# Kernel optimization log

Hardware: AMD Instinct MI355X
Metric: run time of the kernel (lower is better)

## Reference

```python
import jax, jax.numpy as jnp
import numpy as np

K = 1.0          # Lorentz curvature param: x_t^2 - |x_s|^2 = K
SQRT_K = 1.0
EPS = 1e-8
HEADS = 12

def add_time(s):
    t = jnp.sqrt(K + jnp.sum(s * s, axis=-1, keepdims=True))
    return jnp.concatenate([t, s], axis=-1)

def lorentz_ln(x, g, b):
    s = x[..., 1:]
    mu = jnp.mean(s, axis=-1, keepdims=True)
    var = jnp.var(s, axis=-1, keepdims=True)
    s = (s - mu) / jnp.sqrt(var + 1e-5) * g + b
    return add_time(s)

def lorentz_fc(x, W, heads=None, act=None):
    # linear on full Lorentz vector -> space part; time recomputed to stay on manifold
    s = x @ W.T
    if act is not None:
        s = act(s)
    if heads is not None:
        bsz, n, dt = s.shape
        s = s.reshape(bsz, n, heads, dt // heads).transpose(0, 2, 1, 3)  # (b,h,n,hd)
    return add_time(s)

def logmap0(x):
    t, s = x[..., :1], x[..., 1:]
    sn = jnp.sqrt(jnp.sum(s * s, axis=-1, keepdims=True))
    dist = SQRT_K * jnp.arccosh(jnp.maximum(t / SQRT_K, 1.0 + 1e-7))
    u = dist * s / jnp.maximum(sn, EPS)
    return jnp.concatenate([jnp.zeros_like(t), u], axis=-1)

def expmap0(u):
    us = u[..., 1:]
    n = jnp.sqrt(jnp.sum(us * us, axis=-1, keepdims=True))
    nc = jnp.maximum(n, EPS)
    t = SQRT_K * jnp.cosh(n / SQRT_K)
    s = SQRT_K * jnp.sinh(n / SQRT_K) * us / nc
    return jnp.concatenate([t, s], axis=-1)

def ste_clip(x, lo, hi):
    # straight-through estimator: clamp in fwd, identity grad
    return x + jax.lax.stop_gradient(jnp.clip(x, lo, hi) - x)

def ste_max_clamp(x, hi):
    return x + jax.lax.stop_gradient(jnp.minimum(x, hi) - x)

def mha_last_layer(x, Wq, Wk, Wv, Wo, alpha_raw, tau_raw, lambda_raw):
    q = lorentz_fc(x, Wq, heads=HEADS)   # (b,h,n,hd+1)
    k = lorentz_fc(x, Wk, heads=HEADS)
    v = lorentz_fc(x, Wv, heads=HEADS)
    q_t, q_s = q[..., :1], q[..., 1:]
    k_t, k_s = k[..., :1], k[..., 1:]
    # Lorentzian inner product -> hyperbolic pairwise distances
    inner_QK = -q_t @ jnp.swapaxes(k_t, -1, -2) + jnp.einsum('bhid,bhjd->bhij', q_s, k_s)
    raw_cosh = jnp.maximum(-inner_QK / K, 1.0)                # (b,h,n,n)
    is_self = raw_cosh < 1.0 + 1e-5
    safe_cosh = jnp.where(is_self, 2.0, raw_cosh)
    dist_QK = SQRT_K * jnp.arccosh(safe_cosh)
    cosh_OQ = jnp.maximum(q_t / SQRT_K, 1.0 + 1e-7)
    cosh_OK = jnp.maximum(k_t / SQRT_K, 1.0 + 1e-7)
    c_tilde = jnp.minimum(SQRT_K * jnp.arccosh(cosh_OQ), 40.0) / SQRT_K  # (b,h,n,1)
    sinh_QK = jnp.sinh(dist_QK / SQRT_K)
    sinh_OQ = jnp.sinh(c_tilde)
    numer = raw_cosh * cosh_OQ - jnp.swapaxes(cosh_OK, -1, -2)
    raw_Z = numer / (sinh_OQ * sinh_QK)
    Z_safe = jnp.where(is_self, 1.0, ste_clip(raw_Z, -1.0, 1.0))
    alpha = jax.nn.softplus(alpha_raw)
    B = alpha * c_tilde / (1.0 + alpha * c_tilde)
    lam = jax.nn.softplus(lambda_raw)
    d_L = ste_max_clamp(dist_QK, 40.0)   # float32 branch of STE_Dist_Clamp
    log_dist_penalty = -lam * jnp.log1p(d_L * d_L)
    m = 0.1
    entail = jax.nn.softplus(B + Z_safe - m) - jax.nn.softplus(jnp.asarray(-m, B.dtype))
    tau = jax.nn.softplus(tau_raw)
    score = jax.nn.softmax(log_dist_penalty - tau * entail, axis=-1)
    # expmap aggregation: tangent-space weighted mean
    v_tan = logmap0(v)
    agg = jnp.einsum('bhij,bhjd->bhid', score, v_tan)
    agg = agg / (jnp.sum(score, axis=-1, keepdims=True) + 1e-8)
    attn = expmap0(agg).transpose(0, 2, 1, 3)   # (b,n,h,hd+1)
    bsz, n, h, _ = attn.shape
    attn_s = attn[..., 1:].reshape(bsz, n, -1)
    attn_t = attn[..., :1].reshape(bsz, n, -1)
    t_new = jnp.sqrt(jnp.sum(attn_t ** 2, axis=-1, keepdims=True) - (h - 1) * K)
    return lorentz_fc(jnp.concatenate([t_new, attn_s], axis=-1), Wo)


def setup_inputs() -> dict:
    key = jax.random.key(0)
    ks = jax.random.split(key, 8)
    b, n, hidden, mlp_hidden = 4, 1024, 769, 3073
    d = hidden - 1
    xs = jax.random.normal(ks[0], (b, n, d), jnp.float32)
    x = add_time(xs)
    def w(k, o, i):
        return jax.random.normal(k, (o, i), jnp.float32) * (i ** -0.5)
    return {
        'x': x,
        'Wq': w(ks[1], d, hidden), 'Wk': w(ks[2], d, hidden), 'Wv': w(ks[3], d, hidden),
        'Wo': w(ks[4], d, hidden),
        'ln1_g': jnp.ones((d,), jnp.float32), 'ln1_b': jnp.zeros((d,), jnp.float32),
        'ln2_g': jnp.ones((d,), jnp.float32), 'ln2_b': jnp.zeros((d,), jnp.float32),
        'Wm1': w(ks[5], mlp_hidden - 1, hidden), 'Wm2': w(ks[6], d, mlp_hidden),
        'alpha_raw': jnp.zeros((1,), jnp.float32),
        'tau_raw': jnp.zeros((1,), jnp.float32),
        'lambda_raw': jnp.zeros((1,), jnp.float32),
    }


def reference(x, Wq, Wk, Wv, Wo, ln1_g, ln1_b, ln2_g, ln2_b, Wm1, Wm2, alpha_raw, tau_raw, lambda_raw):
    out = mha_last_layer(lorentz_ln(x, ln1_g, ln1_b), Wq, Wk, Wv, Wo, alpha_raw, tau_raw, lambda_raw)
    out = out[..., 1:] + x[..., 1:]                 # residual on space part (DropPath=identity in eval)
    h = lorentz_ln(add_time(out), ln2_g, ln2_b)
    h = lorentz_fc(h, Wm1, act=lambda z: jax.nn.gelu(z, approximate=False))
    h = lorentz_fc(h, Wm2)
    out = h[..., 1:] + out
    return add_time(out)
```

## Files before the change

kernel.cpp:

```cpp
#include <hip/hip_runtime.h>
#include <cstdint>
#include <cstddef>

typedef unsigned short u16;
typedef __attribute__((ext_vector_type(8))) __bf16 bf16x8;
typedef __attribute__((ext_vector_type(4))) float f32x4;
typedef __attribute__((ext_vector_type(4))) short s16x4;

#define SEQ 1024
#define MROWS 4096
#define DDIM 768
#define HID 769
#define KP1 800
#define MLPD 3072
#define KP2 3104
#define NHEADS 12
#define LN2F 0.69314718056f
#define LOG2EF 1.44269504089f

static __device__ __forceinline__ u16 f2bf(float f){
  union { float f; uint32_t u; } v; v.f = f;
  return (u16)((v.u + 0x7FFFu + ((v.u >> 16) & 1u)) >> 16);
}

static __device__ __forceinline__ f32x4 mfma16(bf16x8 a, bf16x8 b, f32x4 c){
  return __builtin_amdgcn_mfma_f32_16x16x32_bf16(a, b, c, 0, 0, 0);
}

static __device__ __forceinline__ f32x4 mfma16k(s16x4 a, s16x4 b, f32x4 c){
  return __builtin_amdgcn_mfma_f32_16x16x16bf16_1k(a, b, c, 0, 0, 0);
}

static __device__ __forceinline__ s16x4 pack4(uint32_t lo, uint32_t hi){
  union { uint2 u; s16x4 v; } cv; cv.u.x = lo; cv.u.y = hi; return cv.v;
}

static __device__ __forceinline__ void async_lds16(const u16* g, u16* l){
  u16* gm = const_cast<u16*>(g);
  __builtin_amdgcn_global_load_lds(
      (__attribute__((address_space(1))) void*)gm,
      (__attribute__((address_space(3))) void*)l, 16, 0, 0);
}

static __device__ __forceinline__ float blk_reduce(float v, float* red, int tid){
  #pragma unroll
  for (int off = 1; off < 64; off <<= 1) v += __shfl_xor(v, off, 64);
  __syncthreads();
  if ((tid & 63) == 0) red[tid >> 6] = v;
  __syncthreads();
  return red[0] + red[1] + red[2] + red[3];
}

static __device__ __forceinline__ float gelu_fast(float z){
  float z2 = z * z;
  float t = __builtin_fmaf(z2, 0.044715f, 1.f);
  float w = z * t * (-2.3022078f);
  float e2 = __builtin_amdgcn_exp2f(w);
  return z * __builtin_amdgcn_rcpf(1.f + e2);
}

static __device__ __forceinline__ void conv_seg(const float* W, u16* O, int idx, int K, int Kp){
  int n = idx / Kp, k = idx - n * Kp;
  O[idx] = (k < K) ? f2bf(W[(size_t)n * K + k]) : (u16)0;
}
__global__ __launch_bounds__(256) void conv_all(const float* __restrict__ Wq, const float* __restrict__ Wk,
    const float* __restrict__ Wv, const float* __restrict__ Wo,
    const float* __restrict__ Wm1, const float* __restrict__ Wm2, u16* __restrict__ dst){
  int b = blockIdx.x, tid = threadIdx.x;
  if (b < 2400){        conv_seg(Wq,  dst,            b*256+tid,        769, 800); }
  else if (b < 4800){   conv_seg(Wk,  dst + 614400,  (b-2400)*256+tid,  769, 800); }
  else if (b < 7200){   conv_seg(Wv,  dst + 1228800, (b-4800)*256+tid,  769, 800); }
  else if (b < 9600){   conv_seg(Wo,  dst + 1843200, (b-7200)*256+tid,  769, 800); }
  else if (b < 19200){  conv_seg(Wm1, dst + 2457600, (b-9600)*256+tid,  769, 800); }
  else {                conv_seg(Wm2, dst + 4915200, (b-19200)*256+tid, 3073, 3104); }
}

__global__ __launch_bounds__(256) void ln_kernel(const float* __restrict__ X, int xstr, int xoff,
    const float* __restrict__ g, const float* __restrict__ b, u16* __restrict__ O){
  __shared__ float red[4];
  int m = blockIdx.x, tid = threadIdx.x;
  const float* xr = X + (size_t)m * xstr + xoff;
  float s[3], y[3];
  float s1 = 0.f, s2 = 0.f;
  #pragma unroll
  for (int j = 0; j < 3; j++){ float v = xr[tid + j*256]; s[j] = v; s1 += v; s2 += v*v; }
  s1 = blk_reduce(s1, red, tid);
  s2 = blk_reduce(s2, red, tid);
  float mu = s1 * (1.f/768.f);
  float var = s2 * (1.f/768.f) - mu*mu;
  float rstd = rsqrtf(var + 1e-5f);
  float q = 0.f;
  #pragma unroll
  for (int j = 0; j < 3; j++){ int i = tid + j*256; y[j] = (s[j]-mu)*rstd*g[i] + b[i]; q += y[j]*y[j]; }
  q = blk_reduce(q, red, tid);
  u16* orow = O + (size_t)m * KP1;
  #pragma unroll
  for (int j = 0; j < 3; j++) orow[1 + tid + j*256] = f2bf(y[j]);
  if (tid == 0) orow[0] = f2bf(sqrtf(1.f + q));
  if (tid < 31) orow[769 + tid] = 0;
}

__global__ __launch_bounds__(256) void ln_sum_kernel(const float* __restrict__ P2,
    const float* __restrict__ x, const float* __restrict__ g, const float* __restrict__ b,
    float* __restrict__ out1, u16* __restrict__ O, float* __restrict__ rsq){
  __shared__ float red[4];
  int m = blockIdx.x, tid = threadIdx.x;
  if (tid == 0) rsq[m] = 0.f;
  float s[3], y[3];
  float s1 = 0.f, s2 = 0.f;
  #pragma unroll
  for (int j = 0; j < 3; j++){
    int col = tid + j*256;
    float v = x[(size_t)m * HID + 1 + col];
    #pragma unroll
    for (int z = 0; z < 2; z++) v += P2[(size_t)z*MROWS*DDIM + (size_t)m*DDIM + col];
    out1[(size_t)m*DDIM + col] = v;
    s[j] = v; s1 += v; s2 += v*v;
  }
  s1 = blk_reduce(s1, red, tid);
  s2 = blk_reduce(s2, red, tid);
  float mu = s1 * (1.f/768.f);
  float var = s2 * (1.f/768.f) - mu*mu;
  float rstd = rsqrtf(var + 1e-5f);
  float q = 0.f;
  #pragma unroll
  for (int j = 0; j < 3; j++){ int i = tid + j*256; y[j] = (s[j]-mu)*rstd*g[i] + b[i]; q += y[j]*y[j]; }
  q = blk_reduce(q, red, tid);
  u16* orow = O + (size_t)m * KP1;
  #pragma unroll
  for (int j = 0; j < 3; j++) orow[1 + tid + j*256] = f2bf(y[j]);
  if (tid == 0) orow[0] = f2bf(sqrtf(1.f + q));
  if (tid < 31) orow[769 + tid] = 0;
}

__global__ __launch_bounds__(256) void gemm_split(
    const u16* __restrict__ A, const u16* __restrict__ B, float* __restrict__ C,
    int N, int Kp)
{
  __shared__ u16 As[128*32];
  __shared__ u16 Bs[128*32];
  int tid = threadIdx.x;
  int wave = tid >> 6, lane = tid & 63;
  int lrow = lane & 15, lq = lane >> 4;
  int m0 = blockIdx.y * 128, n0 = blockIdx.x * 128;
  int wm = wave >> 1, wn = wave & 1;
  int chunks = Kp >> 5;
  int nz = gridDim.z, z = blockIdx.z;
  int base = chunks / nz, rem = chunks - base * nz;
  int begin = z * base + (z < rem ? z : rem);
  int count = base + (z < rem ? 1 : 0);
  C += (size_t)z * MROWS * N;
  f32x4 acc[4][4] = {};
  int seg = wave * 2;
  int srow = lane >> 2;
  int scol = (lane & 3) * 8;
  const u16* Abase = A + (size_t)m0 * Kp;
  const u16* Bbase = B + (size_t)n0 * Kp;
  for (int kc = begin; kc < begin + count; kc++){
    int k0 = kc * 32;
    __syncthreads();
    #pragma unroll
    for (int i = 0; i < 2; i++){
      int s = seg + i;
      async_lds16(Abase + (size_t)(s*16 + srow) * Kp + k0 + scol, As + s*512);
      async_lds16(Bbase + (size_t)(s*16 + srow) * Kp + k0 + scol, Bs + s*512);
    }
    __syncthreads();
    bf16x8 af[4], bfr[4];
    #pragma unroll
    for (int t = 0; t < 4; t++){
      af[t]  = *(const bf16x8*)(As + (wm*64 + t*16 + lrow)*32 + lq*8);
      bfr[t] = *(const bf16x8*)(Bs + (wn*64 + t*16 + lrow)*32 + lq*8);
    }
    #pragma unroll
    for (int mt = 0; mt < 4; mt++)
      #pragma unroll
      for (int nt = 0; nt < 4; nt++)
        acc[mt][nt] = mfma16(af[mt], bfr[nt], acc[mt][nt]);
  }
  #pragma unroll
  for (int mt = 0; mt < 4; mt++)
    #pragma unroll
    for (int nt = 0; nt < 4; nt++){
      int col = n0 + wn*64 + nt*16 + lrow;
      #pragma unroll
      for (int r = 0; r < 4; r++){
        int row = m0 + wm*64 + mt*16 + lq*4 + r;
        C[(size_t)row * N + col] = acc[mt][nt][r];
      }
    }
}

__global__ __launch_bounds__(256) void gemm64(
    const u16* __restrict__ A, const u16* __restrict__ B,
    float* __restrict__ C, u16* __restrict__ Og, float* __restrict__ rsq,
    int N, int Kp, int gelu)
{
  __shared__ u16 As[128*32];
  __shared__ u16 Bs[64*32];
  int tid = threadIdx.x;
  int wave = tid >> 6, lane = tid & 63;
  int lrow = lane & 15, lq = lane >> 4;
  int m0 = blockIdx.y * 128, n0 = blockIdx.x * 64;
  int wm = wave >> 1, wn = wave & 1;
  int chunks = Kp >> 5;
  int nz = gridDim.z, z = blockIdx.z;
  int base = chunks / nz, rem = chunks - base * nz;
  int begin = z * base + (z < rem ? z : rem);
  int count = base + (z < rem ? 1 : 0);
  f32x4 acc[4][2] = {};
  int srow = lane >> 2;
  int scol = (lane & 3) * 8;
  const u16* Abase = A + (size_t)m0 * Kp;
  const u16* Bbase = B + (size_t)n0 * Kp;
  for (int kc = begin; kc < begin + count; kc++){
    int k0 = kc * 32;
    __syncthreads();
    #pragma unroll
    for (int i = 0; i < 2; i++){
      int s = wave*2 + i;
      async_lds16(Abase + (size_t)(s*16 + srow) * Kp + k0 + scol, As + s*512);
    }
    async_lds16(Bbase + (size_t)(wave*16 + srow) * Kp + k0 + scol, Bs + wave*512);
    __syncthreads();
    bf16x8 af[4], bfr[2];
    #pragma unroll
    for (int t = 0; t < 4; t++)
      af[t]  = *(const bf16x8*)(As + (wm*64 + t*16 + lrow)*32 + lq*8);
    #pragma unroll
    for (int t = 0; t < 2; t++)
      bfr[t] = *(const bf16x8*)(Bs + (wn*32 + t*16 + lrow)*32 + lq*8);
    #pragma unroll
    for (int mt = 0; mt < 4; mt++)
      #pragma unroll
      for (int nt = 0; nt < 2; nt++)
        acc[mt][nt] = mfma16(af[mt], bfr[nt], acc[mt][nt]);
  }
  if (gelu == 0){
    C += (size_t)z * MROWS * N;
    #pragma unroll
    for (int mt = 0; mt < 4; mt++)
      #pragma unroll
      for (int nt = 0; nt < 2; nt++){
        int col = n0 + wn*32 + nt*16 + lrow;
        #pragma unroll
        for (int r = 0; r < 4; r++){
          int row = m0 + wm*64 + mt*16 + lq*4 + r;
          C[(size_t)row * N + col] = acc[mt][nt][r];
        }
      }
  } else {
    float ssq[4][4];
    #pragma unroll
    for (int mt = 0; mt < 4; mt++)
      #pragma unroll
      for (int r = 0; r < 4; r++) ssq[mt][r] = 0.f;
    #pragma unroll
    for (int mt = 0; mt < 4; mt++)
      #pragma unroll
      for (int nt = 0; nt < 2; nt++){
        int col = n0 + wn*32 + nt*16 + lrow;
        #pragma unroll
        for (int r = 0; r < 4; r++){
          int row = m0 + wm*64 + mt*16 + lq*4 + r;
          float e = gelu_fast(acc[mt][nt][r]);
          ssq[mt][r] += e*e;
          Og[(size_t)row * KP2 + 1 + col] = f2bf(e);
        }
      }
    #pragma unroll
    for (int mt = 0; mt < 4; mt++)
      #pragma unroll
      for (int r = 0; r < 4; r++){
        float v = ssq[mt][r];
        v += __shfl_xor(v, 1, 64);
        v += __shfl_xor(v, 2, 64);
        v += __shfl_xor(v, 4, 64);
        v += __shfl_xor(v, 8, 64);
        if (lrow == 0)
          atomicAdd(rsq + m0 + wm*64 + mt*16 + lq*4 + r, v);
      }
  }
}

__global__ __launch_bounds__(256) void timecol(const float* __restrict__ rsq, u16* __restrict__ O){
  int idx = blockIdx.x * 256 + threadIdx.x;
  int m = idx >> 5, j = idx & 31;
  if (j == 0) O[(size_t)m * KP2] = f2bf(sqrtf(1.f + rsq[m]));
  else        O[(size_t)m * KP2 + 3072 + j] = 0;
}

__global__ __launch_bounds__(256) void pack_qk(const float* __restrict__ raw,
    u16* __restrict__ Qp, u16* __restrict__ Kpk, float* __restrict__ qt, float* __restrict__ kt)
{
  int wave = threadIdx.x >> 6, lane = threadIdx.x & 63;
  int m = blockIdx.x * 4 + wave;
  int h = blockIdx.y;
  int which = blockIdx.z;
  const float* src = raw + (size_t)m * 2304 + which * 768 + h*64 + lane;
  float v = *src;
  float ss = v*v;
  #pragma unroll
  for (int off = 1; off < 64; off <<= 1) ss += __shfl_xor(ss, off, 64);
  int b = m >> 10, n = m & 1023, bh = b * NHEADS + h;
  u16* dst = (which ? Kpk : Qp) + ((size_t)bh * SEQ + n) * 64 + lane;
  *dst = f2bf(v);
  if (lane == 0) (which ? kt : qt)[bh * SEQ + n] = sqrtf(1.f + ss);
}

__global__ __launch_bounds__(256) void pack_v(const float* __restrict__ vraw, u16* __restrict__ Vf){
  __shared__ float part[256];
  __shared__ float scl[64];
  __shared__ float tile[64][65];
  int tid = threadIdx.x;
  int kb = blockIdx.x, bh = blockIdx.y;
  int b = bh / NHEADS, h = bh - b*NHEADS;
  int kl = tid >> 2;
  int d0 = (tid & 3) * 16;
  int m = b * SEQ + kb * 64 + kl;
  float v[16]; float ss = 0.f;
  const float* src = vraw + (size_t)m * 2304 + h*64 + d0;
  #pragma unroll
  for (int i = 0; i < 16; i++){ v[i] = src[i]; ss += v[i]*v[i]; }
  part[tid] = ss;
  __syncthreads();
  if ((tid & 3) == 0){
    float s2 = part[tid] + part[tid+1] + part[tid+2] + part[tid+3];
    float sn = sqrtf(s2);
    float tv = sqrtf(1.f + s2);
    float ctv = fmaxf(tv, 1.f + 1e-7f);
    float dist = __logf(ctv + sqrtf(fmaxf(ctv*ctv - 1.f, 0.f)));
    scl[kl] = dist / fmaxf(sn, 1e-8f);
  }
  __syncthreads();
  float sc = scl[kl];
  #pragma unroll
  for (int i = 0; i < 16; i++) tile[kl][d0 + i] = v[i] * sc;
  __syncthreads();
  #pragma unroll
  for (int i = 0; i < 2; i++){
    int idx = tid + i*256;
    int ctg_l = idx >> 7;
    int ntp = (idx >> 6) & 1;
    int ln  = idx & 63;
    int lr = ln & 15, lqq = ln >> 4;
    int k0 = ctg_l*16 + lqq*4;
    int dlo = ntp*32 + lr;
    u16 tmp[8];
    #pragma unroll
    for (int j = 0; j < 4; j++){
      tmp[j]     = f2bf(tile[k0+j][dlo]);
      tmp[4+j]   = f2bf(tile[k0+j][dlo+16]);
    }
    u16* dst = Vf + ((((size_t)bh*64 + kb*4 + ctg_l)*2 + ntp)*64 + ln)*8;
    *(uint4*)dst = *(const uint4*)tmp;
  }
}

__global__ __launch_bounds__(256) void attn_kernel(
    const u16* __restrict__ Q, const u16* __restrict__ K, const u16* __restrict__ Vf,
    const float* __restrict__ qt, const float* __restrict__ kt,
    float* __restrict__ pAgg, float* __restrict__ pDen,
    const float* __restrict__ a_raw, const float* __restrict__ t_raw, const float* __restrict__ l_raw)
{
  __shared__ float rv[4][64];
  int tid = threadIdx.x;
  int bh = blockIdx.y, ks = blockIdx.z;
  int qbase = blockIdx.x * 64;
  float alpha = __logf(1.f + __expf(a_raw[0]));
  float tau   = __logf(1.f + __expf(t_raw[0]));
  float lam   = __logf(1.f + __expf(l_raw[0]));
  if (tid < 64){
    float qtv = qt[bh * SEQ + qbase + tid];
    float cq = fmaxf(qtv, 1.f + 1e-7f);
    float A = cq + __builtin_amdgcn_sqrtf(fmaxf(cq*cq - 1.f, 0.f));
    float ct = fminf(__builtin_amdgcn_logf(A) * LN2F, 40.f);
    float e = __expf(ct);
    float sh = 0.5f * (e - __builtin_amdgcn_rcpf(e));
    float ac = alpha * ct;
    rv[0][tid] = qtv;
    rv[1][tid] = cq;
    rv[2][tid] = __builtin_amdgcn_rcpf(sh);
    rv[3][tid] = (ac * __builtin_amdgcn_rcpf(1.f + ac) - 0.1f) * LOG2EF;
  }
  __syncthreads();
  int wave = tid >> 6, lane = tid & 63;
  int lrow = lane & 15, lq = lane >> 4;
  int myrow = wave*16 + lrow;
  float qt_l = rv[0][myrow], cq_l = rv[1][myrow], rri_l = rv[2][myrow], Bw_l = rv[3][myrow];
  const float tbase = tau * 0.92967051f;
  const u16* Qb = Q + ((size_t)bh * SEQ + qbase + wave*16 + lrow) * 64 + lq*8;
  bf16x8 bq0 = *(const bf16x8*)Qb;
  bf16x8 bq1 = *(const bf16x8*)(Qb + 32);
  const u16* Kt = K + (size_t)bh * SEQ * 64 + (size_t)(ks*512 + lrow) * 64 + lq*8;
  const u16* Vp = Vf + (size_t)bh * 65536 + (size_t)(ks*32) * 1024 + lane*8;
  const float* ktp = kt + (size_t)bh * SEQ + ks*512 + lq*4;
  s16x4 ones;
  ones[0] = (short)0x3F80; ones[1] = (short)0x3F80; ones[2] = (short)0x3F80; ones[3] = (short)0x3F80;
  f32x4 o[4] = {};
  f32x4 dacc = {};
  for (int jt = 0; jt < 8; jt++){
    bf16x8 vv[8];
    #pragma unroll
    for (int ct = 0; ct < 4; ct++){
      vv[ct*2]   = *(const bf16x8*)(Vp + ct*1024);
      vv[ct*2+1] = *(const bf16x8*)(Vp + ct*1024 + 512);
    }
    float4 kv[4];
    #pragma unroll
    for (int ct = 0; ct < 4; ct++) kv[ct] = *(const float4*)(ktp + ct*16);
    f32x4 s[4];
    #pragma unroll
    for (int ct = 0; ct < 4; ct++){
      bf16x8 a0 = *(const bf16x8*)(Kt + ct*1024);
      bf16x8 a1 = *(const bf16x8*)(Kt + ct*1024 + 32);
      f32x4 z = {0.f, 0.f, 0.f, 0.f};
      z = mfma16(a0, bq0, z);
      z = mfma16(a1, bq1, z);
      s[ct] = z;
    }
    #pragma unroll
    for (int ct = 0; ct < 4; ct++){
      float4 kvv = kv[ct];
      uint32_t pu[4];
      #pragma unroll
      for (int r = 0; r < 4; r++){
        float ktv = (r == 0) ? kvv.x : (r == 1) ? kvv.y : (r == 2) ? kvv.z : kvv.w;
        float c = fmaxf(__builtin_fmaf(qt_l, ktv, -s[ct][r]), 1.f);
        bool self = c < 1.00001f;
        float ce = self ? 2.f : c;
        float cm1 = __builtin_fmaf(ce, ce, -1.f);
        float rs = __builtin_amdgcn_rsqf(cm1);
        float shq = cm1 * rs;
        float d = __builtin_amdgcn_logf(ce + shq) * LN2F;
        float L1 = __builtin_amdgcn_logf(__builtin_fmaf(d, d, 1.f));
        float Z = __builtin_fmaf(ce, cq_l, -ktv) * rri_l * rs;
        Z = fminf(fmaxf(Z, -1.f), 1.f);
        Z = self ? 1.f : Z;
        float w2 = __builtin_fmaf(Z, LOG2EF, Bw_l);
        float ew = __builtin_amdgcn_exp2f(w2);
        float L2 = __builtin_amdgcn_logf(ew + 1.f);
        float logit = __builtin_fmaf(-lam, L1, __builtin_fmaf(-tau, L2, tbase));
        float p = __builtin_amdgcn_exp2f(logit);
        pu[r] = __float_as_uint(p);
      }
      uint32_t lo = __builtin_amdgcn_perm(pu[1], pu[0], 0x07060302u);
      uint32_t hi = __builtin_amdgcn_perm(pu[3], pu[2], 0x07060302u);
      s16x4 pb = pack4(lo, hi);
      union { bf16x8 v8; s16x4 h[2]; } c0, c1;
      c0.v8 = vv[ct*2]; c1.v8 = vv[ct*2+1];
      o[0] = mfma16k(c0.h[0], pb, o[0]);
      o[1] = mfma16k(c0.h[1], pb, o[1]);
      o[2] = mfma16k(c1.h[0], pb, o[2]);
      o[3] = mfma16k(c1.h[1], pb, o[3]);
      dacc = mfma16k(ones, pb, dacc);
    }
    Kt += 4096; Vp += 4096; ktp += 64;
  }
  size_t rowb = (size_t)(ks*48 + bh) * SEQ + qbase + wave*16 + lrow;
  if (lq == 0) pDen[rowb] = dacc[0];
  #pragma unroll
  for (int nt = 0; nt < 4; nt++){
    float4 ov; ov.x = o[nt][0]; ov.y = o[nt][1]; ov.z = o[nt][2]; ov.w = o[nt][3];
    *(float4*)(pAgg + rowb * 64 + nt*16 + lq*4) = ov;
  }
}

__global__ __launch_bounds__(768) void expmap_pack(const float* __restrict__ pAgg,
    const float* __restrict__ pDen, u16* __restrict__ O){
  __shared__ float th2[NHEADS];
  int m = blockIdx.x, tid = threadIdx.x;
  int h = tid >> 6, lane = tid & 63;
  int b = m >> 10, n = m & 1023, bh = b*NHEADS + h;
  size_t i0 = ((size_t)bh * SEQ + n);
  size_t i1 = ((size_t)(48 + bh) * SEQ + n);
  float d = pDen[i0] + pDen[i1];
  float rden = __builtin_amdgcn_rcpf(d * (1.f + 1e-8f));
  float u = (pAgg[i0*64 + lane] + pAgg[i1*64 + lane]) * rden;
  float n2 = u*u;
  #pragma unroll
  for (int off = 1; off < 64; off <<= 1) n2 += __shfl_xor(n2, off, 64);
  float nn = sqrtf(n2);
  float e = __expf(nn);
  float ch = 0.5f * (e + 1.f/e);
  float sh = 0.5f * (e - 1.f/e);
  float sc = sh / fmaxf(nn, 1e-8f);
  u16* orow = O + (size_t)m * KP1;
  orow[1 + h*64 + lane] = f2bf(u * sc);
  if (lane == 0) th2[h] = ch*ch;
  __syncthreads();
  if (tid == 0){
    float ssum = 0.f;
    #pragma unroll
    for (int i = 0; i < NHEADS; i++) ssum += th2[i];
    orow[0] = f2bf(sqrtf(ssum - 11.f));
  }
  if (tid >= 1 && tid < 32) orow[768 + tid] = 0;
}

__global__ __launch_bounds__(256) void final_sum(const float* __restrict__ P4,
    const float* __restrict__ out1, float* __restrict__ out){
  __shared__ float red[4];
  int m = blockIdx.x, tid = threadIdx.x;
  float v[3]; float s2 = 0.f;
  #pragma unroll
  for (int j = 0; j < 3; j++){
    int col = tid + j*256;
    float t = out1[(size_t)m*DDIM + col];
    #pragma unroll
    for (int z = 0; z < 4; z++) t += P4[(size_t)z*MROWS*DDIM + (size_t)m*DDIM + col];
    v[j] = t; s2 += t*t;
  }
  s2 = blk_reduce(s2, red, tid);
  float* orow = out + (size_t)m * HID;
  if (tid == 0) orow[0] = sqrtf(1.f + s2);
  #pragma unroll
  for (int j = 0; j < 3; j++) orow[1 + tid + j*256] = v[j];
}

extern "C" void kernel_launch(void* const* d_in, const int* in_sizes, int n_in,
                              void* d_out, int out_size, void* d_ws, size_t ws_size,
                              hipStream_t stream)
{
  (void)in_sizes; (void)n_in; (void)out_size; (void)ws_size;
  const float* x   = (const float*)d_in[0];
  const float* Wq  = (const float*)d_in[1];
  const float* Wk  = (const float*)d_in[2];
  const float* Wv  = (const float*)d_in[3];
  const float* Wo  = (const float*)d_in[4];
  const float* g1p = (const float*)d_in[5];
  const float* b1p = (const float*)d_in[6];
  const float* g2p = (const float*)d_in[7];
  const float* b2p = (const float*)d_in[8];
  const float* Wm1 = (const float*)d_in[9];
  const float* Wm2 = (const float*)d_in[10];
  const float* ar  = (const float*)d_in[11];
  const float* tr  = (const float*)d_in[12];
  const float* lr  = (const float*)d_in[13];

  char* ws = (char*)d_ws;
  u16*   wqb  = (u16*)(ws + 0);
  u16*   wob  = (u16*)(ws + 3686400);
  u16*   wm1b = (u16*)(ws + 4915200);
  u16*   wm2b = (u16*)(ws + 9830400);
  u16*   xln  = (u16*)(ws + 14598144);
  float* qkv  = (float*)(ws + 21151744);
  u16*   qp   = (u16*)(ws + 58900480);
  u16*   kpk  = (u16*)(ws + 65191936);
  u16*   vf   = (u16*)(ws + 71483392);
  float* rsq  = (float*)(ws + 77774848);
  float* qtb  = (float*)(ws + 77791232);
  float* ktb  = (float*)(ws + 77987840);
  float* pAgg = (float*)(ws + 78381056);
  float* pDen = (float*)(ws + 103546880);
  u16*   woin = (u16*)(ws + 103940096);
  float* woP  = (float*)(ws + 21151744);
  float* out1 = (float*)(ws + 103940096);
  u16*   ln2b = (u16*)(ws + 78381056);
  u16*   g1b  = (u16*)(ws + 21151744);
  float* out2P= (float*)(ws + 46579712);

  conv_all<<<dim3(28512), 256, 0, stream>>>(Wq, Wk, Wv, Wo, Wm1, Wm2, wqb);
  ln_kernel<<<dim3(4096), 256, 0, stream>>>(x, 769, 1, g1p, b1p, xln);
  gemm64<<<dim3(36, 32, 1), 256, 0, stream>>>(xln, wqb, qkv, nullptr, nullptr, 2304, 800, 0);
  pack_qk<<<dim3(1024, 12, 2), 256, 0, stream>>>(qkv, qp, kpk, qtb, ktb);
  pack_v<<<dim3(16, 48), 256, 0, stream>>>(qkv + 1536, vf);
  attn_kernel<<<dim3(16, 48, 2), 256, 0, stream>>>(qp, kpk, vf, qtb, ktb, pAgg, pDen, ar, tr, lr);
  expmap_pack<<<dim3(4096), 768, 0, stream>>>(pAgg, pDen, woin);
  gemm64<<<dim3(12, 32, 2), 256, 0, stream>>>(woin, wob, woP, nullptr, nullptr, 768, 800, 0);
  ln_sum_kernel<<<dim3(4096), 256, 0, stream>>>(woP, x, g2p, b2p, out1, ln2b, rsq);
  gemm64<<<dim3(48, 32, 1), 256, 0, stream>>>(ln2b, wm1b, nullptr, g1b, rsq, 3072, 800, 1);
  timecol<<<dim3(512), 256, 0, stream>>>(rsq, g1b);
  gemm_split<<<dim3(6, 32, 4), 256, 0, stream>>>(g1b, wm2b, out2P, 768, 3104);
  final_sum<<<dim3(4096), 256, 0, stream>>>(out2P, out1, (float*)d_out);
}
```

Measured before the change: 393.6 us.

## Deepen GEMM K-tile to 64 and reuse gemm64 for MLP down-projection

The gemm64 kernel now stages 64-wide K chunks per iteration instead of 32, which halves the number of barrier pairs and doubles the MFMA work between syncs. All padded K dimensions grow to multiples of 64 (832 and 3136), with the padding writes and workspace offsets adjusted to match. The separate 128x128 gemm_split kernel is removed, and the final MLP GEMM now runs on gemm64 with 64-wide N tiles and a 4-way K split. The cost is extra zero-padding work, double the shared memory per block (which may lower occupancy), and smaller N tiles for the last GEMM.

```diff
diff --git a/kernel.cpp b/kernel.cpp
--- a/kernel.cpp
+++ b/kernel.cpp
@@ -11,9 +11,9 @@
 #define MROWS 4096
 #define DDIM 768
 #define HID 769
-#define KP1 800
+#define KP1 832
 #define MLPD 3072
-#define KP2 3104
+#define KP2 3136
 #define NHEADS 12
 #define LN2F 0.69314718056f
 #define LOG2EF 1.44269504089f
@@ -67,12 +67,12 @@
     const float* __restrict__ Wv, const float* __restrict__ Wo,
     const float* __restrict__ Wm1, const float* __restrict__ Wm2, u16* __restrict__ dst){
   int b = blockIdx.x, tid = threadIdx.x;
-  if (b < 2400){        conv_seg(Wq,  dst,            b*256+tid,        769, 800); }
-  else if (b < 4800){   conv_seg(Wk,  dst + 614400,  (b-2400)*256+tid,  769, 800); }
-  else if (b < 7200){   conv_seg(Wv,  dst + 1228800, (b-4800)*256+tid,  769, 800); }
-  else if (b < 9600){   conv_seg(Wo,  dst + 1843200, (b-7200)*256+tid,  769, 800); }
-  else if (b < 19200){  conv_seg(Wm1, dst + 2457600, (b-9600)*256+tid,  769, 800); }
-  else {                conv_seg(Wm2, dst + 4915200, (b-19200)*256+tid, 3073, 3104); }
+  if (b < 2496){        conv_seg(Wq,  dst,            b*256+tid,         769, 832); }
+  else if (b < 4992){   conv_seg(Wk,  dst + 638976,  (b-2496)*256+tid,   769, 832); }
+  else if (b < 7488){   conv_seg(Wv,  dst + 1277952, (b-4992)*256+tid,   769, 832); }
+  else if (b < 9984){   conv_seg(Wo,  dst + 1916928, (b-7488)*256+tid,   769, 832); }
+  else if (b < 19968){  conv_seg(Wm1, dst + 2555904, (b-9984)*256+tid,   769, 832); }
+  else {                conv_seg(Wm2, dst + 5111808, (b-19968)*256+tid, 3073, 3136); }
 }
 
 __global__ __launch_bounds__(256) void ln_kernel(const float* __restrict__ X, int xstr, int xoff,
@@ -97,7 +97,7 @@
   #pragma unroll
   for (int j = 0; j < 3; j++) orow[1 + tid + j*256] = f2bf(y[j]);
   if (tid == 0) orow[0] = f2bf(sqrtf(1.f + q));
-  if (tid < 31) orow[769 + tid] = 0;
+  if (tid < 63) orow[769 + tid] = 0;
 }
 
 __global__ __launch_bounds__(256) void ln_sum_kernel(const float* __restrict__ P2,
@@ -130,65 +130,7 @@
   #pragma unroll
   for (int j = 0; j < 3; j++) orow[1 + tid + j*256] = f2bf(y[j]);
   if (tid == 0) orow[0] = f2bf(sqrtf(1.f + q));
-  if (tid < 31) orow[769 + tid] = 0;
-}
-
-__global__ __launch_bounds__(256) void gemm_split(
-    const u16* __restrict__ A, const u16* __restrict__ B, float* __restrict__ C,
-    int N, int Kp)
-{
-  __shared__ u16 As[128*32];
-  __shared__ u16 Bs[128*32];
-  int tid = threadIdx.x;
-  int wave = tid >> 6, lane = tid & 63;
-  int lrow = lane & 15, lq = lane >> 4;
-  int m0 = blockIdx.y * 128, n0 = blockIdx.x * 128;
-  int wm = wave >> 1, wn = wave & 1;
-  int chunks = Kp >> 5;
-  int nz = gridDim.z, z = blockIdx.z;
-  int base = chunks / nz, rem = chunks - base * nz;
-  int begin = z * base + (z < rem ? z : rem);
-  int count = base + (z < rem ? 1 : 0);
-  C += (size_t)z * MROWS * N;
-  f32x4 acc[4][4] = {};
-  int seg = wave * 2;
-  int srow = lane >> 2;
-  int scol = (lane & 3) * 8;
-  const u16* Abase = A + (size_t)m0 * Kp;
-  const u16* Bbase = B + (size_t)n0 * Kp;
-  for (int kc = begin; kc < begin + count; kc++){
-    int k0 = kc * 32;
-    __syncthreads();
-    #pragma unroll
-    for (int i = 0; i < 2; i++){
-      int s = seg + i;
-      async_lds16(Abase + (size_t)(s*16 + srow) * Kp + k0 + scol, As + s*512);
-      async_lds16(Bbase + (size_t)(s*16 + srow) * Kp + k0 + scol, Bs + s*512);
-    }
-    __syncthreads();
-    bf16x8 af[4], bfr[4];
-    #pragma unroll
-    for (int t = 0; t < 4; t++){
-      af[t]  = *(const bf16x8*)(As + (wm*64 + t*16 + lrow)*32 + lq*8);
-      bfr[t] = *(const bf16x8*)(Bs + (wn*64 + t*16 + lrow)*32 + lq*8);
-    }
-    #pragma unroll
-    for (int mt = 0; mt < 4; mt++)
-      #pragma unroll
-      for (int nt = 0; nt < 4; nt++)
-        acc[mt][nt] = mfma16(af[mt], bfr[nt], acc[mt][nt]);
-  }
-  #pragma unroll
-  for (int mt = 0; mt < 4; mt++)
-    #pragma unroll
-    for (int nt = 0; nt < 4; nt++){
-      int col = n0 + wn*64 + nt*16 + lrow;
-      #pragma unroll
-      for (int r = 0; r < 4; r++){
-        int row = m0 + wm*64 + mt*16 + lq*4 + r;
-        C[(size_t)row * N + col] = acc[mt][nt][r];
-      }
-    }
+  if (tid < 63) orow[769 + tid] = 0;
 }
 
 __global__ __launch_bounds__(256) void gemm64(
@@ -196,45 +138,55 @@
     float* __restrict__ C, u16* __restrict__ Og, float* __restrict__ rsq,
     int N, int Kp, int gelu)
 {
-  __shared__ u16 As[128*32];
-  __shared__ u16 Bs[64*32];
+  __shared__ u16 As[128*64];
+  __shared__ u16 Bs[64*64];
   int tid = threadIdx.x;
   int wave = tid >> 6, lane = tid & 63;
   int lrow = lane & 15, lq = lane >> 4;
   int m0 = blockIdx.y * 128, n0 = blockIdx.x * 64;
   int wm = wave >> 1, wn = wave & 1;
-  int chunks = Kp >> 5;
+  int chunks = Kp >> 6;
   int nz = gridDim.z, z = blockIdx.z;
   int base = chunks / nz, rem = chunks - base * nz;
   int begin = z * base + (z < rem ? z : rem);
   int count = base + (z < rem ? 1 : 0);
   f32x4 acc[4][2] = {};
-  int srow = lane >> 2;
-  int scol = (lane & 3) * 8;
+  int srow = lane >> 3;
+  int scol = (lane & 7) * 8;
   const u16* Abase = A + (size_t)m0 * Kp;
   const u16* Bbase = B + (size_t)n0 * Kp;
   for (int kc = begin; kc < begin + count; kc++){
-    int k0 = kc * 32;
+    int k0 = kc * 64;
     __syncthreads();
+    #pragma unroll
+    for (int i = 0; i < 4; i++){
+      int s = wave*4 + i;
+      async_lds16(Abase + (size_t)(s*8 + srow) * Kp + k0 + scol, As + s*512);
+    }
     #pragma unroll
     for (int i = 0; i < 2; i++){
       int s = wave*2 + i;
-      async_lds16(Abase + (size_t)(s*16 + srow) * Kp + k0 + scol, As + s*512);
+      async_lds16(Bbase + (size_t)(s*8 + srow) * Kp + k0 + scol, Bs + s*512);
     }
-    async_lds16(Bbase + (size_t)(wave*16 + srow) * Kp + k0 + scol, Bs + wave*512);
     __syncthreads();
-    bf16x8 af[4], bfr[2];
+    bf16x8 af[4][2], bfr[2][2];
     #pragma unroll
     for (int t = 0; t < 4; t++)
-      af[t]  = *(const bf16x8*)(As + (wm*64 + t*16 + lrow)*32 + lq*8);
+      #pragma unroll
+      for (int kk = 0; kk < 2; kk++)
+        af[t][kk] = *(const bf16x8*)(As + (wm*64 + t*16 + lrow)*64 + kk*32 + lq*8);
     #pragma unroll
     for (int t = 0; t < 2; t++)
-      bfr[t] = *(const bf16x8*)(Bs + (wn*32 + t*16 + lrow)*32 + lq*8);
-    #pragma unroll
-    for (int mt = 0; mt < 4; mt++)
-      #pragma unroll
-      for (int nt = 0; nt < 2; nt++)
-        acc[mt][nt] = mfma16(af[mt], bfr[nt], acc[mt][nt]);
+      #pragma unroll
+      for (int kk = 0; kk < 2; kk++)
+        bfr[t][kk] = *(const bf16x8*)(Bs + (wn*32 + t*16 + lrow)*64 + kk*32 + lq*8);
+    #pragma unroll
+    for (int kk = 0; kk < 2; kk++)
+      #pragma unroll
+      for (int mt = 0; mt < 4; mt++)
+        #pragma unroll
+        for (int nt = 0; nt < 2; nt++)
+          acc[mt][nt] = mfma16(af[mt][kk], bfr[nt][kk], acc[mt][nt]);
   }
   if (gelu == 0){
     C += (size_t)z * MROWS * N;
@@ -285,7 +237,7 @@
 
 __global__ __launch_bounds__(256) void timecol(const float* __restrict__ rsq, u16* __restrict__ O){
   int idx = blockIdx.x * 256 + threadIdx.x;
-  int m = idx >> 5, j = idx & 31;
+  int m = idx >> 6, j = idx & 63;
   if (j == 0) O[(size_t)m * KP2] = f2bf(sqrtf(1.f + rsq[m]));
   else        O[(size_t)m * KP2 + 3072 + j] = 0;
 }
@@ -495,7 +447,7 @@
     for (int i = 0; i < NHEADS; i++) ssum += th2[i];
     orow[0] = f2bf(sqrtf(ssum - 11.f));
   }
-  if (tid >= 1 && tid < 32) orow[768 + tid] = 0;
+  if (tid >= 1 && tid < 64) orow[768 + tid] = 0;
 }
 
 __global__ __launch_bounds__(256) void final_sum(const float* __restrict__ P4,
@@ -540,37 +492,37 @@
 
   char* ws = (char*)d_ws;
   u16*   wqb  = (u16*)(ws + 0);
-  u16*   wob  = (u16*)(ws + 3686400);
-  u16*   wm1b = (u16*)(ws + 4915200);
-  u16*   wm2b = (u16*)(ws + 9830400);
-  u16*   xln  = (u16*)(ws + 14598144);
-  float* qkv  = (float*)(ws + 21151744);
-  u16*   qp   = (u16*)(ws + 58900480);
-  u16*   kpk  = (u16*)(ws + 65191936);
-  u16*   vf   = (u16*)(ws + 71483392);
-  float* rsq  = (float*)(ws + 77774848);
-  float* qtb  = (float*)(ws + 77791232);
-  float* ktb  = (float*)(ws + 77987840);
-  float* pAgg = (float*)(ws + 78381056);
-  float* pDen = (float*)(ws + 103546880);
-  u16*   woin = (u16*)(ws + 103940096);
-  float* woP  = (float*)(ws + 21151744);
-  float* out1 = (float*)(ws + 103940096);
-  u16*   ln2b = (u16*)(ws + 78381056);
-  u16*   g1b  = (u16*)(ws + 21151744);
-  float* out2P= (float*)(ws + 46579712);
-
-  conv_all<<<dim3(28512), 256, 0, stream>>>(Wq, Wk, Wv, Wo, Wm1, Wm2, wqb);
+  u16*   wob  = (u16*)(ws + 3833856);
+  u16*   wm1b = (u16*)(ws + 5111808);
+  u16*   wm2b = (u16*)(ws + 10223616);
+  u16*   xln  = (u16*)(ws + 15040512);
+  float* qkv  = (float*)(ws + 21856256);
+  u16*   qp   = (u16*)(ws + 59604992);
+  u16*   kpk  = (u16*)(ws + 65896448);
+  u16*   vf   = (u16*)(ws + 72187904);
+  float* rsq  = (float*)(ws + 78479360);
+  float* qtb  = (float*)(ws + 78495744);
+  float* ktb  = (float*)(ws + 78692352);
+  float* pAgg = (float*)(ws + 78888960);
+  float* pDen = (float*)(ws + 104054784);
+  u16*   woin = (u16*)(ws + 104448000);
+  float* woP  = (float*)(ws + 21856256);
+  u16*   ln2b = (u16*)(ws + 78888960);
+  u16*   g1b  = (u16*)(ws + 21856256);
+  float* out2P= (float*)(ws + 47546368);
+  float* out1 = (float*)(ws + 97878016);
+
+  conv_all<<<dim3(29376), 256, 0, stream>>>(Wq, Wk, Wv, Wo, Wm1, Wm2, wqb);
   ln_kernel<<<dim3(4096), 256, 0, stream>>>(x, 769, 1, g1p, b1p, xln);
-  gemm64<<<dim3(36, 32, 1), 256, 0, stream>>>(xln, wqb, qkv, nullptr, nullptr, 2304, 800, 0);
+  gemm64<<<dim3(36, 32, 1), 256, 0, stream>>>(xln, wqb, qkv, nullptr, nullptr, 2304, 832, 0);
   pack_qk<<<dim3(1024, 12, 2), 256, 0, stream>>>(qkv, qp, kpk, qtb, ktb);
   pack_v<<<dim3(16, 48), 256, 0, stream>>>(qkv + 1536, vf);
   attn_kernel<<<dim3(16, 48, 2), 256, 0, stream>>>(qp, kpk, vf, qtb, ktb, pAgg, pDen, ar, tr, lr);
   expmap_pack<<<dim3(4096), 768, 0, stream>>>(pAgg, pDen, woin);
-  gemm64<<<dim3(12, 32, 2), 256, 0, stream>>>(woin, wob, woP, nullptr, nullptr, 768, 800, 0);
+  gemm64<<<dim3(12, 32, 2), 256, 0, stream>>>(woin, wob, woP, nullptr, nullptr, 768, 832, 0);
   ln_sum_kernel<<<dim3(4096), 256, 0, stream>>>(woP, x, g2p, b2p, out1, ln2b, rsq);
-  gemm64<<<dim3(48, 32, 1), 256, 0, stream>>>(ln2b, wm1b, nullptr, g1b, rsq, 3072, 800, 1);
-  timecol<<<dim3(512), 256, 0, stream>>>(rsq, g1b);
-  gemm_split<<<dim3(6, 32, 4), 256, 0, stream>>>(g1b, wm2b, out2P, 768, 3104);
+  gemm64<<<dim3(48, 32, 1), 256, 0, stream>>>(ln2b, wm1b, nullptr, g1b, rsq, 3072, 832, 1);
+  timecol<<<dim3(1024), 256, 0, stream>>>(rsq, g1b);
+  gemm64<<<dim3(12, 32, 4), 256, 0, stream>>>(g1b, wm2b, out2P, nullptr, nullptr, 768, 3136, 0);
   final_sum<<<dim3(4096), 256, 0, stream>>>(out2P, out1, (float*)d_out);
 }
```

New measurement: 396.9 us. About the same (+0.9%).
